# Kernel optimization log

Measured on AMD Instinct MI355X. Metric: run time of the kernel, lower is better.

The kernel has to match this reference:

```python
import jax, jax.numpy as jnp
import numpy as np

B_BOXES = 2          # boxes per cell (b in source)
NUM_CLASSES = 20     # pred channels = B_BOXES*5 + NUM_CLASSES = 30
LAMBDA_COORD = 5.0
LAMBDA_NOOBJ = 0.5


def setup_inputs() -> dict:
    key = jax.random.key(0)
    k1, k2, k3 = jax.random.split(key, 3)
    N, S = 16384, 7
    preds = jax.random.uniform(k1, (N, S, S, B_BOXES * 5 + NUM_CLASSES), dtype=jnp.float32)
    targets = jax.random.uniform(k2, (N, S, S, 5 + NUM_CLASSES), dtype=jnp.float32)
    # channel 0 of target is the object indicator c (checked via c == 1)
    obj = (jax.random.uniform(k3, (N, S, S)) < 0.3).astype(jnp.float32)
    targets = targets.at[..., 0].set(obj)
    return {"preds": preds, "targets": targets}


def reference(preds, targets):
    # preds: [N,S,S,30]; targets: [N,S,S,25]
    N, S1, S2, _ = preds.shape
    bboxes = preds[..., : B_BOXES * 5].reshape(N, S1, S2, B_BOXES, 5)
    obj_scores = bboxes[..., 0]                         # [N,S,S,B]
    idx = jnp.argmax(obj_scores, axis=-1)               # [N,S,S] best box by confidence
    best = jnp.take_along_axis(bboxes, idx[..., None, None], axis=3)[..., 0, :]  # [N,S,S,5]

    c_mask = (targets[..., 0] == 1.0)                   # object present per cell

    box_loss = jnp.sum((best[..., 1:5] - targets[..., 1:5]) ** 2, axis=-1)
    pc_loss = (best[..., 0] - targets[..., 0]) ** 2
    class_loss = jnp.sum((preds[..., B_BOXES * 5:] - targets[..., 5:]) ** 2, axis=-1)

    obj_term = LAMBDA_COORD * box_loss + pc_loss + class_loss
    noobj_term = LAMBDA_NOOBJ * jnp.sum(obj_scores ** 2, axis=-1)

    loss = jnp.sum(jnp.where(c_mask, obj_term, noobj_term))
    return loss
```

## Files before the change

### kernel.cpp

```cpp
#include <hip/hip_runtime.h>

#define LAMBDA_COORD 5.0f
#define LAMBDA_NOOBJ 0.5f


typedef float f4u __attribute__((ext_vector_type(4), aligned(4)));
typedef float f2u __attribute__((ext_vector_type(2), aligned(4)));

__global__ void zero_out_kernel(float* out, int n) {
    int i = blockIdx.x * blockDim.x + threadIdx.x;
    if (i < n) out[i] = 0.0f;
}

__global__ __launch_bounds__(256, 6) void yolo_loss_kernel(
    const float* __restrict__ preds, const float* __restrict__ targets,
    float* __restrict__ ws, int n_cells)
{
    __shared__ float s_part[4];
    const int tid = threadIdx.x;
    const int c = blockIdx.x * 256 + tid;

    float loss = 0.0f;
    if (c < n_cells) {
        const float* pbase = preds + (size_t)c * 30;
        const float* tbase = targets + (size_t)c * 25;
        const f4u* pp = (const f4u*)pbase;
        const f4u* tp = (const f4u*)tbase;

        f4u P0 = pp[0], P1 = pp[1], P2 = pp[2], P3 = pp[3];
        f4u P4 = pp[4], P5 = pp[5], P6 = pp[6];
        f2u P7 = *(const f2u*)(pbase + 28);
        f4u T0 = tp[0], T1 = tp[1], T2 = tp[2], T3 = tp[3];
        f4u T4 = tp[4], T5 = tp[5];
        float t24 = tbase[24];

        float p0 = P0.x, p5c = P1.y;
        bool pick1 = p5c > p0;
        float b0 = pick1 ? p5c  : p0;
        float b1 = pick1 ? P1.z : P0.y;
        float b2 = pick1 ? P1.w : P0.z;
        float b3 = pick1 ? P2.x : P0.w;
        float b4 = pick1 ? P2.y : P1.x;

        float t0 = T0.x;
        float d1 = b1 - T0.y, d2 = b2 - T0.z, d3 = b3 - T0.w, d4 = b4 - T1.x;
        float box_loss = d1 * d1 + d2 * d2 + d3 * d3 + d4 * d4;
        float dpc = b0 - t0;
        float pc_loss = dpc * dpc;

        float cl = 0.0f, d;
        d = P2.z - T1.y; cl += d * d;
        d = P2.w - T1.z; cl += d * d;
        d = P3.x - T1.w; cl += d * d;
        d = P3.y - T2.x; cl += d * d;
        d = P3.z - T2.y; cl += d * d;
        d = P3.w - T2.z; cl += d * d;
        d = P4.x - T2.w; cl += d * d;
        d = P4.y - T3.x; cl += d * d;
        d = P4.z - T3.y; cl += d * d;
        d = P4.w - T3.z; cl += d * d;
        d = P5.x - T3.w; cl += d * d;
        d = P5.y - T4.x; cl += d * d;
        d = P5.z - T4.y; cl += d * d;
        d = P5.w - T4.z; cl += d * d;
        d = P6.x - T4.w; cl += d * d;
        d = P6.y - T5.x; cl += d * d;
        d = P6.z - T5.y; cl += d * d;
        d = P6.w - T5.z; cl += d * d;
        d = P7.x - T5.w; cl += d * d;
        d = P7.y - t24;  cl += d * d;

        float obj_term = LAMBDA_COORD * box_loss + pc_loss + cl;
        float noobj_term = LAMBDA_NOOBJ * (p0 * p0 + p5c * p5c);
        loss = (t0 == 1.0f) ? obj_term : noobj_term;
    }

    #pragma unroll
    for (int off = 32; off > 0; off >>= 1)
        loss += __shfl_down(loss, off, 64);

    const int wave = tid >> 6;
    if ((tid & 63) == 0) s_part[wave] = loss;
    __syncthreads();
    if (tid == 0) {
        ws[blockIdx.x] = s_part[0] + s_part[1] + s_part[2] + s_part[3];
    }
}

__global__ __launch_bounds__(256) void reduce_ws_kernel(
    const float* __restrict__ ws, float* __restrict__ out, int n)
{
    __shared__ float s_part[4];
    const int tid = threadIdx.x;

    float s = 0.0f;
    for (int i = tid; i < n; i += 256) s += ws[i];

    #pragma unroll
    for (int off = 32; off > 0; off >>= 1)
        s += __shfl_down(s, off, 64);

    const int wave = tid >> 6;
    if ((tid & 63) == 0) s_part[wave] = s;
    __syncthreads();
    if (tid == 0)
        out[0] = s_part[0] + s_part[1] + s_part[2] + s_part[3];
}

extern "C" void kernel_launch(void* const* d_in, const int* in_sizes, int n_in,
                              void* d_out, int out_size, void* d_ws, size_t ws_size,
                              hipStream_t stream) {
    const float* preds   = (const float*)d_in[0];
    const float* targets = (const float*)d_in[1];
    float* out = (float*)d_out;
    float* ws  = (float*)d_ws;

    const int n_cells = in_sizes[0] / 30;
    const int grid = (n_cells + 255) / 256;

    zero_out_kernel<<<(out_size + 255) / 256, 256, 0, stream>>>(out, out_size);

    yolo_loss_kernel<<<grid, 256, 0, stream>>>(preds, targets, ws, n_cells);
    reduce_ws_kernel<<<1, 256, 0, stream>>>(ws, out, grid);
}
```

Measured before the change: 197.4 us.

## Stage cell chunks through LDS with coalesced float4 loads and register prefetch

Replaces the one-cell-per-thread strided loads with a persistent grid of 1024 blocks. Each block streams 128-cell chunks into LDS using fully coalesced float4 loads, prefetches the next chunk into registers while computing the current one, and has half the threads compute cell losses from shared memory. The leftover tail cells are folded into the final single-block reduction kernel. The aim is better coalescing and overlap of load with compute. The costs are extra LDS traffic, an extra barrier per chunk, half the threads idle during compute, and possible LDS bank conflicts from the 30- and 25-float strides.

```diff
diff --git a/kernel.cpp b/kernel.cpp
--- a/kernel.cpp
+++ b/kernel.cpp
@@ -2,8 +2,11 @@
 
 #define LAMBDA_COORD 5.0f
 #define LAMBDA_NOOBJ 0.5f
-
-
+#define NBLK 1024
+#define CHUNK 128
+
+
+typedef float f4 __attribute__((ext_vector_type(4)));
 typedef float f4u __attribute__((ext_vector_type(4), aligned(4)));
 typedef float f2u __attribute__((ext_vector_type(2), aligned(4)));
 
@@ -12,15 +15,111 @@
     if (i < n) out[i] = 0.0f;
 }
 
-__global__ __launch_bounds__(256, 6) void yolo_loss_kernel(
+__device__ __forceinline__ float cell_loss(const float* __restrict__ P,
+                                           const float* __restrict__ T) {
+    float q0 = P[0], q1 = P[1], q2 = P[2], q3 = P[3], q4 = P[4];
+    float q5 = P[5], q6 = P[6], q7 = P[7], q8 = P[8], q9 = P[9];
+
+    bool pick1 = q5 > q0;
+    float b0 = pick1 ? q5 : q0;
+    float b1 = pick1 ? q6 : q1;
+    float b2 = pick1 ? q7 : q2;
+    float b3 = pick1 ? q8 : q3;
+    float b4 = pick1 ? q9 : q4;
+
+    float t0 = T[0];
+    float d1 = b1 - T[1], d2 = b2 - T[2], d3 = b3 - T[3], d4 = b4 - T[4];
+    float box_loss = d1 * d1 + d2 * d2 + d3 * d3 + d4 * d4;
+    float dpc = b0 - t0;
+    float pc_loss = dpc * dpc;
+
+    float cl = 0.0f;
+    #pragma unroll
+    for (int k = 0; k < 20; ++k) {
+        float d = P[10 + k] - T[5 + k];
+        cl += d * d;
+    }
+
+    float obj_term = LAMBDA_COORD * box_loss + pc_loss + cl;
+    float noobj_term = LAMBDA_NOOBJ * (q0 * q0 + q5 * q5);
+    return (t0 == 1.0f) ? obj_term : noobj_term;
+}
+
+__global__ __launch_bounds__(256, 4) void yolo_loss_kernel(
     const float* __restrict__ preds, const float* __restrict__ targets,
-    float* __restrict__ ws, int n_cells)
+    float* __restrict__ ws, int nchunk)
+{
+    __shared__ float sp[CHUNK * 30];
+    __shared__ float st[CHUNK * 25];
+    __shared__ float s_part[4];
+
+    const int tid = threadIdx.x;
+    const int stride = gridDim.x;
+    f4* sp4 = (f4*)sp;
+    f4* st4 = (f4*)st;
+
+    float acc = 0.0f;
+    int g = blockIdx.x;
+
+    if (g < nchunk) {
+        f4 a0, a1, a2, a3, b0, b1, b2, b3;
+        {
+            const f4* pg = (const f4*)(preds + (size_t)g * (CHUNK * 30));
+            const f4* tg = (const f4*)(targets + (size_t)g * (CHUNK * 25));
+            a0 = pg[tid]; a1 = pg[tid + 256]; a2 = pg[tid + 512];
+            if (tid < 192) a3 = pg[tid + 768];
+            b0 = tg[tid]; b1 = tg[tid + 256]; b2 = tg[tid + 512];
+            if (tid < 32) b3 = tg[tid + 768];
+        }
+
+        for (;;) {
+            sp4[tid] = a0; sp4[tid + 256] = a1; sp4[tid + 512] = a2;
+            if (tid < 192) sp4[tid + 768] = a3;
+            st4[tid] = b0; st4[tid + 256] = b1; st4[tid + 512] = b2;
+            if (tid < 32) st4[tid + 768] = b3;
+            __syncthreads();
+
+            const int gn = g + stride;
+            const bool more = gn < nchunk;
+            if (more) {
+                const f4* pg = (const f4*)(preds + (size_t)gn * (CHUNK * 30));
+                const f4* tg = (const f4*)(targets + (size_t)gn * (CHUNK * 25));
+                a0 = pg[tid]; a1 = pg[tid + 256]; a2 = pg[tid + 512];
+                if (tid < 192) a3 = pg[tid + 768];
+                b0 = tg[tid]; b1 = tg[tid + 256]; b2 = tg[tid + 512];
+                if (tid < 32) b3 = tg[tid + 768];
+            }
+
+            if (tid < CHUNK)
+                acc += cell_loss(sp + tid * 30, st + tid * 25);
+
+            if (!more) break;
+            __syncthreads();
+            g = gn;
+        }
+    }
+
+    #pragma unroll
+    for (int off = 32; off > 0; off >>= 1)
+        acc += __shfl_down(acc, off, 64);
+    if ((tid & 63) == 0) s_part[tid >> 6] = acc;
+    __syncthreads();
+    if (tid == 0)
+        ws[blockIdx.x] = s_part[0] + s_part[1] + s_part[2] + s_part[3];
+}
+
+__global__ __launch_bounds__(256) void reduce_ws_kernel(
+    const float* __restrict__ ws,
+    const float* __restrict__ preds, const float* __restrict__ targets,
+    float* __restrict__ out, int nblk, int tail_start, int n_cells)
 {
     __shared__ float s_part[4];
     const int tid = threadIdx.x;
-    const int c = blockIdx.x * 256 + tid;
-
-    float loss = 0.0f;
+
+    float s = 0.0f;
+    for (int i = tid; i < nblk; i += 256) s += ws[i];
+
+    const int c = tail_start + tid;
     if (c < n_cells) {
         const float* pbase = preds + (size_t)c * 30;
         const float* tbase = targets + (size_t)c * 25;
@@ -72,36 +171,13 @@
 
         float obj_term = LAMBDA_COORD * box_loss + pc_loss + cl;
         float noobj_term = LAMBDA_NOOBJ * (p0 * p0 + p5c * p5c);
-        loss = (t0 == 1.0f) ? obj_term : noobj_term;
+        s += (t0 == 1.0f) ? obj_term : noobj_term;
     }
-
-    #pragma unroll
-    for (int off = 32; off > 0; off >>= 1)
-        loss += __shfl_down(loss, off, 64);
-
-    const int wave = tid >> 6;
-    if ((tid & 63) == 0) s_part[wave] = loss;
-    __syncthreads();
-    if (tid == 0) {
-        ws[blockIdx.x] = s_part[0] + s_part[1] + s_part[2] + s_part[3];
-    }
-}
-
-__global__ __launch_bounds__(256) void reduce_ws_kernel(
-    const float* __restrict__ ws, float* __restrict__ out, int n)
-{
-    __shared__ float s_part[4];
-    const int tid = threadIdx.x;
-
-    float s = 0.0f;
-    for (int i = tid; i < n; i += 256) s += ws[i];
 
     #pragma unroll
     for (int off = 32; off > 0; off >>= 1)
         s += __shfl_down(s, off, 64);
-
-    const int wave = tid >> 6;
-    if ((tid & 63) == 0) s_part[wave] = s;
+    if ((tid & 63) == 0) s_part[tid >> 6] = s;
     __syncthreads();
     if (tid == 0)
         out[0] = s_part[0] + s_part[1] + s_part[2] + s_part[3];
@@ -116,10 +192,14 @@
     float* ws  = (float*)d_ws;
 
     const int n_cells = in_sizes[0] / 30;
-    const int grid = (n_cells + 255) / 256;
+    const int nchunk = n_cells / CHUNK;
+    const int tail_start = nchunk * CHUNK;
 
     zero_out_kernel<<<(out_size + 255) / 256, 256, 0, stream>>>(out, out_size);
 
-    yolo_loss_kernel<<<grid, 256, 0, stream>>>(preds, targets, ws, n_cells);
-    reduce_ws_kernel<<<1, 256, 0, stream>>>(ws, out, grid);
-}
+    int grid = NBLK;
+    if (grid > nchunk) grid = nchunk;
+    yolo_loss_kernel<<<grid, 256, 0, stream>>>(preds, targets, ws, nchunk);
+    reduce_ws_kernel<<<1, 256, 0, stream>>>(ws, preds, targets, out,
+                                            grid, tail_start, n_cells);
+}
```

After: 197.6 us. About the same (+0.1%).
